# Performance work log

Measured on AMD Instinct MI355X. Metric: run time of the kernel, lower is better.

Reference implementation:

```python
import jax, jax.numpy as jnp
import numpy as np

N, S, E, H = 4, 4096, 1024, 16
D = E // H  # 64


def setup_inputs() -> dict:
    key = jax.random.key(0)
    ks = jax.random.split(key, 6)
    scale = 0.02
    x = jax.random.normal(ks[0], (N, S, E), dtype=jnp.float32)
    Wq = jax.random.normal(ks[1], (E, E), dtype=jnp.float32) * scale
    Wk = jax.random.normal(ks[2], (E, E), dtype=jnp.float32) * scale
    Wv = jax.random.normal(ks[3], (E, E), dtype=jnp.float32) * scale
    Wo = jax.random.normal(ks[4], (E, E), dtype=jnp.float32) * scale
    bo = jax.random.normal(ks[5], (E,), dtype=jnp.float32) * scale
    return {"x": x, "Wq": Wq, "Wk": Wk, "Wv": Wv, "Wo": Wo, "bo": bo}


def reference(x, Wq, Wk, Wv, Wo, bo):
    n, s, _ = x.shape
    # torch nn.Linear(bias=False): y = x @ W.T  (W stored as [out, in])
    q = (x @ Wq.T).reshape(n, s, H, D).transpose(0, 2, 1, 3)  # (N, H, S, D)
    k = (x @ Wk.T).reshape(n, s, H, D).transpose(0, 2, 1, 3)  # (N, H, S, D)
    v = (x @ Wv.T).reshape(n, s, H, D).transpose(0, 2, 1, 3)  # (N, H, S, D)
    # Faithful to source: einsum subscripts applied to the PERMUTED (N,H,S,D)
    # tensors, so label q->H, h->S. energy: (N, H, H, S)
    energy = jnp.einsum('nqhd,nkhd->nqkh', q, k)
    attention = jax.nn.softmax(energy / (D ** 0.5), axis=3)
    # 'nqkh,nvhd->nqhd': k and v are independently summed free indices
    out = jnp.einsum('nqkh,nvhd->nqhd', attention, v).reshape(n, s, E)  # (N,S,E)
    return out @ Wo.T + bo
```

## Files before the change

### kernel.cpp

```cpp
#include <hip/hip_runtime.h>
#include <stdint.h>

typedef unsigned short u16;
typedef unsigned int   u32;
typedef __attribute__((ext_vector_type(8))) short short8;
typedef __attribute__((ext_vector_type(4))) float f32x4;
typedef __attribute__((ext_vector_type(8))) u16   u16x8;

static constexpr size_t NX = (size_t)4 * 4096 * 1024;
static constexpr size_t NW = (size_t)1024 * 1024;

static constexpr size_t OFF_XB   = 0;
static constexpr size_t OFF_EN   = 0;
static constexpr size_t OFF_QK   = 33554432;
static constexpr size_t OFF_WQB  = 100663296;
static constexpr size_t OFF_WKB  = 102760448;
static constexpr size_t OFF_WOB  = 104857600;
static constexpr size_t OFF_WVST = 106954752;
static constexpr size_t OFF_VS   = 107216896;
static constexpr size_t OFF_GMAX = 111411200;
static constexpr size_t OFF_INVZ = 111415296;
static constexpr size_t OFF_ST   = 111419392;

static __device__ __forceinline__ u16 f2bf(float f) {
    u32 u = __builtin_bit_cast(u32, f);
    u += 0x7fffu + ((u >> 16) & 1u);
    return (u16)(u >> 16);
}
static __device__ __forceinline__ float bf2f(u16 v) {
    u32 u = ((u32)v) << 16;
    return __builtin_bit_cast(float, u);
}

#if __has_builtin(__builtin_amdgcn_global_load_lds)
#define HAVE_GLOAD_LDS 1
static __device__ __forceinline__ void gload_lds16(const void* g, void* l) {
    __builtin_amdgcn_global_load_lds(
        (__attribute__((address_space(1))) void*)(uintptr_t)g,
        (__attribute__((address_space(3))) void*)(uintptr_t)l,
        16, 0, 0);
}
#endif

#if __has_builtin(__builtin_amdgcn_sched_barrier)
#define SCHED_FENCE() __builtin_amdgcn_sched_barrier(0)
#else
#define SCHED_FENCE()
#endif

__global__ __launch_bounds__(256)
void cvt_kernel(const float* __restrict__ x, const float* __restrict__ wq,
                const float* __restrict__ wk, const float* __restrict__ wo,
                u16* __restrict__ xb, u16* __restrict__ wqb,
                u16* __restrict__ wkb, u16* __restrict__ wob)
{
    size_t i = ((size_t)blockIdx.x * 256 + threadIdx.x) * 8;
    const float* s; u16* dst; size_t o;
    if (i < NX) { s = x; dst = xb; o = i; }
    else {
        size_t r = i - NX;
        int w = (int)(r >> 20);
        o = r & (NW - 1);
        s   = (w == 0) ? wq  : (w == 1) ? wk  : wo;
        dst = (w == 0) ? wqb : (w == 1) ? wkb : wob;
    }
    f32x4 a = *(const f32x4*)&s[o];
    f32x4 c = *(const f32x4*)&s[o + 4];
    u16x8 v;
    v[0]=f2bf(a[0]); v[1]=f2bf(a[1]); v[2]=f2bf(a[2]); v[3]=f2bf(a[3]);
    v[4]=f2bf(c[0]); v[5]=f2bf(c[1]); v[6]=f2bf(c[2]); v[7]=f2bf(c[3]);
    *(u16x8*)&dst[o] = v;
}

__global__ __launch_bounds__(256)
void wvst_kernel(const float* __restrict__ Wv, u16* __restrict__ Bvs)
{
    int idx = blockIdx.x * 256 + threadIdx.x;
    int d = idx >> 10;
    int e = idx & 1023;
    float s = 0.f;
    #pragma unroll
    for (int h = 0; h < 16; ++h) s += Wv[(size_t)(h * 64 + d) * 1024 + e];
    Bvs[(size_t)d * 1024 + e] = f2bf(s);
}

__global__ __launch_bounds__(512, 2)
void gemm_qk(const u16* __restrict__ A, const u16* __restrict__ Bw,
             u16* __restrict__ C, int M, int N, int K, int lognbx)
{
    __shared__ u16 lds[65536];
    const int tid  = threadIdx.x;
    const int wave = tid >> 6;
    const int lane = tid & 63;

    const int nwg = gridDim.x;
    const int swz = ((int)blockIdx.x & 7) * (nwg >> 3) + ((int)blockIdx.x >> 3);
    const long col0 = (long)(swz & ((1 << lognbx) - 1)) * 256;
    const long row0 = (long)(swz >> lognbx) * 256;

    const int wr2 = wave >> 2;
    const int wc2 = wave & 3;
    const int fr  = lane & 15;
    const int kq  = lane >> 4;
    const int rxor = fr & 7;

    const int t255  = tid & 255;
    const int halfA = tid >> 8;
    const int gAsrc = (t255 & 7) ^ ((t255 >> 3) & 7);
    const u16* sA = A + (size_t)(row0 + halfA * 128 + (t255 >> 3)) * K + gAsrc * 8;
    const int dA = halfA * 8192 + t255 * 8;

    const int u  = (tid & 127) | ((tid >> 1) & 128);
    const int bh = (tid >> 7) & 1;
    const int gBsrc = (u & 7) ^ ((u >> 3) & 7);
    const u16* sB = Bw + (size_t)(col0 + bh * 128 + (u >> 3)) * K + gBsrc * 8;
    const int dB = bh * 8192 + u * 8;

    auto STAGE = [&](int buf, int k0) {
        #pragma unroll
        for (int l = 0; l < 4; ++l) {
#ifdef HAVE_GLOAD_LDS
            gload_lds16(sA + (size_t)l * 32 * K + k0, &lds[buf * 16384 + dA + l * 2048]);
            gload_lds16(sB + (size_t)l * 32 * K + k0, &lds[32768 + buf * 16384 + dB + l * 2048]);
#else
            *(short8*)&lds[buf * 16384 + dA + l * 2048] =
                *(const short8*)(sA + (size_t)l * 32 * K + k0);
            *(short8*)&lds[32768 + buf * 16384 + dB + l * 2048] =
                *(const short8*)(sB + (size_t)l * 32 * K + k0);
#endif
        }
    };

    f32x4 acc[8][4] = {};

    STAGE(0, 0);
    __syncthreads();

    const int nt = K >> 6;
    for (int t = 0; t < nt; ++t) {
        const int cur = t & 1;
        const int base  = cur * 16384;
        const int bbase = 32768 + cur * 16384;

        short8 af[4][2], bf[4][2];
        #pragma unroll
        for (int m = 0; m < 4; ++m) {
            const int row = wr2 * 128 + m * 16 + fr;
            #pragma unroll
            for (int kk = 0; kk < 2; ++kk)
                af[m][kk] = *(const short8*)&lds[base + row * 64 + (((kk << 2) | kq) ^ rxor) * 8];
        }
        #pragma unroll
        for (int n = 0; n < 4; ++n) {
            const int col = wc2 * 64 + n * 16 + fr;
            #pragma unroll
            for (int kk = 0; kk < 2; ++kk)
                bf[n][kk] = *(const short8*)&lds[bbase + col * 64 + (((kk << 2) | kq) ^ rxor) * 8];
        }
        if (t + 1 < nt) STAGE(cur ^ 1, (t + 1) << 6);
        SCHED_FENCE();
        __builtin_amdgcn_s_barrier();

        __builtin_amdgcn_s_setprio(1);
        #pragma unroll
        for (int kk = 0; kk < 2; ++kk)
            #pragma unroll
            for (int m = 0; m < 4; ++m)
                #pragma unroll
                for (int n = 0; n < 2; ++n)
                    acc[m][n] = __builtin_amdgcn_mfma_f32_16x16x32_bf16(af[m][kk], bf[n][kk], acc[m][n], 0, 0, 0);
        __builtin_amdgcn_s_setprio(0);
        __builtin_amdgcn_s_barrier();

        __builtin_amdgcn_s_setprio(1);
        #pragma unroll
        for (int kk = 0; kk < 2; ++kk)
            #pragma unroll
            for (int m = 0; m < 4; ++m)
                #pragma unroll
                for (int n = 2; n < 4; ++n)
                    acc[m][n] = __builtin_amdgcn_mfma_f32_16x16x32_bf16(af[m][kk], bf[n][kk], acc[m][n], 0, 0, 0);
        __builtin_amdgcn_s_setprio(0);

        short8 ag[4][2];
        #pragma unroll
        for (int m = 0; m < 4; ++m) {
            const int row = wr2 * 128 + 64 + m * 16 + fr;
            #pragma unroll
            for (int kk = 0; kk < 2; ++kk)
                ag[m][kk] = *(const short8*)&lds[base + row * 64 + (((kk << 2) | kq) ^ rxor) * 8];
        }
        SCHED_FENCE();
        __builtin_amdgcn_s_barrier();

        __builtin_amdgcn_s_setprio(1);
        #pragma unroll
        for (int kk = 0; kk < 2; ++kk)
            #pragma unroll
            for (int m = 0; m < 4; ++m)
                #pragma unroll
                for (int n = 0; n < 2; ++n)
                    acc[m + 4][n] = __builtin_amdgcn_mfma_f32_16x16x32_bf16(ag[m][kk], bf[n][kk], acc[m + 4][n], 0, 0, 0);
        __builtin_amdgcn_s_setprio(0);
        __builtin_amdgcn_s_barrier();

        __builtin_amdgcn_s_setprio(1);
        #pragma unroll
        for (int kk = 0; kk < 2; ++kk)
            #pragma unroll
            for (int m = 0; m < 4; ++m)
                #pragma unroll
                for (int n = 2; n < 4; ++n)
                    acc[m + 4][n] = __builtin_amdgcn_mfma_f32_16x16x32_bf16(ag[m][kk], bf[n][kk], acc[m + 4][n], 0, 0, 0);
        __builtin_amdgcn_s_setprio(0);

        __syncthreads();
    }

    #pragma unroll
    for (int m = 0; m < 8; ++m) {
        #pragma unroll
        for (int n = 0; n < 4; ++n) {
            long gr = row0 + wr2 * 128 + m * 16 + kq * 4;
            long gc = col0 + wc2 * 64 + n * 16 + fr;
            #pragma unroll
            for (int j = 0; j < 4; ++j)
                C[(gr + j) * N + gc] = f2bf(acc[m][n][j]);
        }
    }
}

__global__ __launch_bounds__(256)
void gemm_vs(const u16* __restrict__ A, const u16* __restrict__ Bw,
             u16* __restrict__ C)
{
    __shared__ u16 lsA[2][64 * 32];
    __shared__ u16 lsB[2][64 * 32];
    const int tid  = threadIdx.x;
    const int wave = tid >> 6;
    const int lane = tid & 63;
    const long row0 = (long)blockIdx.x * 64;
    const int wr = (wave >> 1) * 32;
    const int wc = (wave & 1) * 32;
    const int fr = lane & 15;
    const int k8 = (lane >> 4) * 8;

    f32x4 acc[2][2] = {};
    const int c0 = tid;
    const u16* pa = &A [(row0 + (c0 >> 2)) * 1024 + (c0 & 3) * 8];
    const u16* pb = &Bw[((size_t)(c0 >> 2)) * 1024 + (c0 & 3) * 8];

    auto STAGE = [&](int buf, int k0) {
#ifdef HAVE_GLOAD_LDS
        gload_lds16(pa + k0, &lsA[buf][wave * 512]);
        gload_lds16(pb + k0, &lsB[buf][wave * 512]);
#else
        *(short8*)&lsA[buf][(size_t)c0 * 8] = *(const short8*)(pa + k0);
        *(short8*)&lsB[buf][(size_t)c0 * 8] = *(const short8*)(pb + k0);
#endif
    };

    STAGE(0, 0);
    __syncthreads();
    for (int t = 0; t < 32; ++t) {
        const int cur = t & 1;
        if (t + 1 < 32) STAGE(cur ^ 1, (t + 1) << 5);
        short8 af[2], bf[2];
        #pragma unroll
        for (int m = 0; m < 2; ++m)
            af[m] = *(const short8*)&lsA[cur][(wr + m * 16 + fr) * 32 + k8];
        #pragma unroll
        for (int n = 0; n < 2; ++n)
            bf[n] = *(const short8*)&lsB[cur][(wc + n * 16 + fr) * 32 + k8];
        #pragma unroll
        for (int m = 0; m < 2; ++m)
            #pragma unroll
            for (int n = 0; n < 2; ++n)
                acc[m][n] = __builtin_amdgcn_mfma_f32_16x16x32_bf16(af[m], bf[n], acc[m][n], 0, 0, 0);
        __syncthreads();
    }

    const int orow = (lane >> 4) * 4;
    #pragma unroll
    for (int m = 0; m < 2; ++m) {
        #pragma unroll
        for (int n = 0; n < 2; ++n) {
            long gr = row0 + wr + m * 16 + orow;
            int  gc = wc + n * 16 + fr;
            #pragma unroll
            for (int j = 0; j < 4; ++j)
                C[(gr + j) * 64 + gc] = f2bf(acc[m][n][j]);
        }
    }
}

__global__ __launch_bounds__(256)
void energy_kernel(const u16* __restrict__ QKb, float* __restrict__ E)
{
    const int lane = threadIdx.x & 63;
    const size_t site = (size_t)blockIdx.x * 4 + (threadIdx.x >> 6);
    const u16* qrow = QKb + site * 2048;
    const int hh = lane & 15;
    const int kg = (lane >> 4) * 8;
    short8 a0 = *(const short8*)&qrow[hh * 64 + kg];
    short8 a1 = *(const short8*)&qrow[hh * 64 + 32 + kg];
    short8 b0 = *(const short8*)&qrow[1024 + hh * 64 + kg];
    short8 b1 = *(const short8*)&qrow[1024 + hh * 64 + 32 + kg];
    f32x4 acc = {};
    acc = __builtin_amdgcn_mfma_f32_16x16x32_bf16(a0, b0, acc, 0, 0, 0);
    acc = __builtin_amdgcn_mfma_f32_16x16x32_bf16(a1, b1, acc, 0, 0, 0);
    float* out = E + site * 256;
    const int ib = (lane >> 4) * 4;
    #pragma unroll
    for (int r = 0; r < 4; ++r)
        out[(ib + r) * 16 + hh] = acc[r];
}

__global__ __launch_bounds__(256)
void stats_part(const float* __restrict__ E, float* __restrict__ pmax,
                float* __restrict__ psum)
{
    const int b = blockIdx.x, p = threadIdx.x;
    const float* e = E + (size_t)b * 64 * 256 + p;
    float m = -3.4e38f;
    float buf[64];
    #pragma unroll 8
    for (int s = 0; s < 64; ++s) {
        float v = e[(size_t)s * 256];
        buf[s] = v;
        m = fmaxf(m, v);
    }
    float z = 0.f;
    #pragma unroll 8
    for (int s = 0; s < 64; ++s) z += __expf((buf[s] - m) * 0.125f);
    pmax[b * 256 + p] = m;
    psum[b * 256 + p] = z;
}
__global__ __launch_bounds__(256)
void stats_comb(const float* __restrict__ pmax, const float* __restrict__ psum,
                float* __restrict__ gmax, float* __restrict__ invZ)
{
    const int n = blockIdx.x, p = threadIdx.x;
    float m = -3.4e38f;
    #pragma unroll 8
    for (int c = 0; c < 64; ++c) m = fmaxf(m, pmax[(n * 64 + c) * 256 + p]);
    float z = 0.f;
    #pragma unroll 8
    for (int c = 0; c < 64; ++c)
        z += psum[(n * 64 + c) * 256 + p] * __expf((pmax[(n * 64 + c) * 256 + p] - m) * 0.125f);
    gmax[n * 256 + p] = m;
    invZ[n * 256 + p] = 1.0f / z;
}

__global__ __launch_bounds__(256)
void g_kernel(const u16* __restrict__ Vsb, const u16* __restrict__ Wob,
              float* __restrict__ G)
{
    __shared__ u16 lA[64 * 64];
    __shared__ u16 lB[256 * 64];
    const int tid = threadIdx.x;
    const int wave = tid >> 6, lane = tid & 63;
    const int op = blockIdx.x, uc = blockIdx.y, sl = blockIdx.z;

    {
        const int j = tid >> 2;
        const size_t srow = (size_t)16 * (64 * uc + j) + sl;
        #pragma unroll
        for (int h = 0; h < 2; ++h) {
            const int g = (tid & 3) + h * 4;
            u16x8 v = *(const u16x8*)&Vsb[srow * 64 + g * 8];
            *(u16x8*)&lA[j * 64 + ((g ^ (j & 7)) * 8)] = v;
        }
    }
    {
        const size_t o = (size_t)op * 256 + tid;
        #pragma unroll
        for (int g = 0; g < 8; ++g) {
            u16x8 v = *(const u16x8*)&Wob[o * 1024 + 64 * sl + g * 8];
            *(u16x8*)&lB[tid * 64 + ((g ^ (tid & 7)) * 8)] = v;
        }
    }
    __syncthreads();

    const int fr = lane & 15, kq = lane >> 4;
    f32x4 acc[4][4] = {};
    #pragma unroll
    for (int kk = 0; kk < 2; ++kk) {
        short8 af[4], bq[4];
        #pragma unroll
        for (int m = 0; m < 4; ++m) {
            const int j = m * 16 + fr;
            af[m] = *(const short8*)&lA[j * 64 + (((kq + 4 * kk) ^ (j & 7)) * 8)];
        }
        #pragma unroll
        for (int n = 0; n < 4; ++n) {
            const int o = wave * 64 + n * 16 + fr;
            bq[n] = *(const short8*)&lB[o * 64 + (((kq + 4 * kk) ^ (o & 7)) * 8)];
        }
        #pragma unroll
        for (int m = 0; m < 4; ++m)
            #pragma unroll
            for (int n = 0; n < 4; ++n)
                acc[m][n] = __builtin_amdgcn_mfma_f32_16x16x32_bf16(af[m], bq[n], acc[m][n], 0, 0, 0);
    }

    #pragma unroll
    for (int m = 0; m < 4; ++m) {
        #pragma unroll
        for (int n = 0; n < 4; ++n) {
            const int ocol = op * 256 + wave * 64 + n * 16 + fr;
            #pragma unroll
            for (int jj = 0; jj < 4; ++jj) {
                const int j = m * 16 + kq * 4 + jj;
                G[((size_t)16 * (64 * uc + j) + sl) * 1024 + ocol] = acc[m][n][jj];
            }
        }
    }
}

__global__ __launch_bounds__(256)
void comb_kernel(const float* __restrict__ En, const float* __restrict__ gmax,
                 const float* __restrict__ invZ, const float* __restrict__ G,
                 const float* __restrict__ bo, float* __restrict__ out)
{
    __shared__ float sm[256], sz[256], sa[256];
    const int b = blockIdx.x;
    const int n = b >> 8, c = b & 255;
    const int t = threadIdx.x;
    sm[t] = gmax[n * 256 + t];
    sz[t] = invZ[n * 256 + t];
    __syncthreads();
    {
        const int sl = t >> 4, i = t & 15;
        const float* e = En + ((size_t)n * 4096 + c * 16 + sl) * 256 + i * 16;
        float a = 0.f;
        #pragma unroll
        for (int j = 0; j < 16; ++j)
            a += __expf((e[j] - sm[i * 16 + j]) * 0.125f) * sz[i * 16 + j];
        sa[sl * 16 + i] = a;
    }
    __syncthreads();

    const int o0 = t * 4;
    const float* gp = G + ((size_t)n * 4096 + c * 16) * 1024 + o0;
    f32x4 g[16];
    #pragma unroll
    for (int sl = 0; sl < 16; ++sl) g[sl] = *(const f32x4*)&gp[(size_t)sl * 1024];
    const f32x4 b4 = *(const f32x4*)&bo[o0];
    #pragma unroll
    for (int i = 0; i < 16; ++i) {
        f32x4 acc = b4;
        #pragma unroll
        for (int sl = 0; sl < 16; ++sl) {
            const float a = sa[sl * 16 + i];
            acc[0] += a * g[sl][0];
            acc[1] += a * g[sl][1];
            acc[2] += a * g[sl][2];
            acc[3] += a * g[sl][3];
        }
        *(f32x4*)&out[((size_t)n * 4096 + i * 256 + c) * 1024 + o0] = acc;
    }
}

extern "C" void kernel_launch(void* const* d_in, const int* in_sizes, int n_in,
                              void* d_out, int out_size, void* d_ws, size_t ws_size,
                              hipStream_t stream)
{
    const float* x  = (const float*)d_in[0];
    const float* Wq = (const float*)d_in[1];
    const float* Wk = (const float*)d_in[2];
    const float* Wv = (const float*)d_in[3];
    const float* Wo = (const float*)d_in[4];
    const float* bo = (const float*)d_in[5];
    float* out = (float*)d_out;
    char* ws = (char*)d_ws;

    u16*   xb   = (u16*)  (ws + OFF_XB);
    float* En   = (float*)(ws + OFF_EN);
    u16*   QKb  = (u16*)  (ws + OFF_QK);
    float* G    = (float*)(ws + OFF_QK);
    u16*   Wqb  = (u16*)  (ws + OFF_WQB);
    u16*   Wkb  = (u16*)  (ws + OFF_WKB);
    u16*   Wob  = (u16*)  (ws + OFF_WOB);
    u16*   Bvs  = (u16*)  (ws + OFF_WVST);
    u16*   Vsb  = (u16*)  (ws + OFF_VS);
    float* gmax = (float*)(ws + OFF_GMAX);
    float* invZ = (float*)(ws + OFF_INVZ);
    float* pmax = (float*)(ws + OFF_ST);
    float* psum = (float*)(ws + OFF_ST + 262144);

    cvt_kernel <<<9728, 256, 0, stream>>>(x, Wq, Wk, Wo, xb, Wqb, Wkb, Wob);
    wvst_kernel<<<256,  256, 0, stream>>>(Wv, Bvs);

    gemm_qk<<<512, 512, 0, stream>>>(xb, Wqb, QKb, 16384, 2048, 1024, 3);
    gemm_vs<<<256, 256, 0, stream>>>(xb, Bvs, Vsb);

    energy_kernel<<<4096, 256, 0, stream>>>(QKb, En);

    stats_part<<<256, 256, 0, stream>>>(En, pmax, psum);
    stats_comb<<<4,   256, 0, stream>>>(pmax, psum, gmax, invZ);

    g_kernel<<<dim3(4, 16, 16), 256, 0, stream>>>(Vsb, Wob, G);

    comb_kernel<<<1024, 256, 0, stream>>>(En, gmax, invZ, G, bo, out);
}
```

Baseline: 185.3 us.

## Store G intermediate in bf16 and drop intra-iteration barriers in QK GEMM

The G matrix (attention-weight by Wo product) is now written as bf16 instead of fp32 and converted back in the combine kernel, halving the write and read traffic of this large intermediate. Separately, the QK GEMM main loop issues the next-tile prefetch first, loads all A and B fragments up front, and removes the per-quarter s_barrier synchronisations, reordering the MFMAs into three groups. This trades some accuracy in G and higher register pressure in the GEMM for less memory traffic and fewer barriers.

Result: faster. 179.7 us (-3.0%).

```diff
diff --git a/kernel.cpp b/kernel.cpp
--- a/kernel.cpp
+++ b/kernel.cpp
@@ -6,6 +6,7 @@
 typedef __attribute__((ext_vector_type(8))) short short8;
 typedef __attribute__((ext_vector_type(4))) float f32x4;
 typedef __attribute__((ext_vector_type(8))) u16   u16x8;
+typedef __attribute__((ext_vector_type(4))) u16   u16x4;
 
 static constexpr size_t NX = (size_t)4 * 4096 * 1024;
 static constexpr size_t NW = (size_t)1024 * 1024;
@@ -142,7 +143,9 @@
         const int base  = cur * 16384;
         const int bbase = 32768 + cur * 16384;
 
-        short8 af[4][2], bf[4][2];
+        if (t + 1 < nt) STAGE(cur ^ 1, (t + 1) << 6);
+
+        short8 af[4][2], ag[4][2], bf[2][2], bg[2][2];
         #pragma unroll
         for (int m = 0; m < 4; ++m) {
             const int row = wr2 * 128 + m * 16 + fr;
@@ -151,15 +154,20 @@
                 af[m][kk] = *(const short8*)&lds[base + row * 64 + (((kk << 2) | kq) ^ rxor) * 8];
         }
         #pragma unroll
-        for (int n = 0; n < 4; ++n) {
+        for (int n = 0; n < 2; ++n) {
             const int col = wc2 * 64 + n * 16 + fr;
             #pragma unroll
             for (int kk = 0; kk < 2; ++kk)
                 bf[n][kk] = *(const short8*)&lds[bbase + col * 64 + (((kk << 2) | kq) ^ rxor) * 8];
         }
-        if (t + 1 < nt) STAGE(cur ^ 1, (t + 1) << 6);
+        #pragma unroll
+        for (int m = 0; m < 4; ++m) {
+            const int row = wr2 * 128 + 64 + m * 16 + fr;
+            #pragma unroll
+            for (int kk = 0; kk < 2; ++kk)
+                ag[m][kk] = *(const short8*)&lds[base + row * 64 + (((kk << 2) | kq) ^ rxor) * 8];
+        }
         SCHED_FENCE();
-        __builtin_amdgcn_s_barrier();
 
         __builtin_amdgcn_s_setprio(1);
         #pragma unroll
@@ -170,28 +178,15 @@
                 for (int n = 0; n < 2; ++n)
                     acc[m][n] = __builtin_amdgcn_mfma_f32_16x16x32_bf16(af[m][kk], bf[n][kk], acc[m][n], 0, 0, 0);
         __builtin_amdgcn_s_setprio(0);
-        __builtin_amdgcn_s_barrier();
-
-        __builtin_amdgcn_s_setprio(1);
-        #pragma unroll
-        for (int kk = 0; kk < 2; ++kk)
-            #pragma unroll
-            for (int m = 0; m < 4; ++m)
-                #pragma unroll
-                for (int n = 2; n < 4; ++n)
-                    acc[m][n] = __builtin_amdgcn_mfma_f32_16x16x32_bf16(af[m][kk], bf[n][kk], acc[m][n], 0, 0, 0);
-        __builtin_amdgcn_s_setprio(0);
-
-        short8 ag[4][2];
-        #pragma unroll
-        for (int m = 0; m < 4; ++m) {
-            const int row = wr2 * 128 + 64 + m * 16 + fr;
+
+        #pragma unroll
+        for (int n = 0; n < 2; ++n) {
+            const int col = wc2 * 64 + (n + 2) * 16 + fr;
             #pragma unroll
             for (int kk = 0; kk < 2; ++kk)
-                ag[m][kk] = *(const short8*)&lds[base + row * 64 + (((kk << 2) | kq) ^ rxor) * 8];
+                bg[n][kk] = *(const short8*)&lds[bbase + col * 64 + (((kk << 2) | kq) ^ rxor) * 8];
         }
         SCHED_FENCE();
-        __builtin_amdgcn_s_barrier();
 
         __builtin_amdgcn_s_setprio(1);
         #pragma unroll
@@ -201,17 +196,20 @@
                 #pragma unroll
                 for (int n = 0; n < 2; ++n)
                     acc[m + 4][n] = __builtin_amdgcn_mfma_f32_16x16x32_bf16(ag[m][kk], bf[n][kk], acc[m + 4][n], 0, 0, 0);
-        __builtin_amdgcn_s_setprio(0);
-        __builtin_amdgcn_s_barrier();
-
-        __builtin_amdgcn_s_setprio(1);
         #pragma unroll
         for (int kk = 0; kk < 2; ++kk)
             #pragma unroll
             for (int m = 0; m < 4; ++m)
                 #pragma unroll
-                for (int n = 2; n < 4; ++n)
-                    acc[m + 4][n] = __builtin_amdgcn_mfma_f32_16x16x32_bf16(ag[m][kk], bf[n][kk], acc[m + 4][n], 0, 0, 0);
+                for (int n = 0; n < 2; ++n)
+                    acc[m][n + 2] = __builtin_amdgcn_mfma_f32_16x16x32_bf16(af[m][kk], bg[n][kk], acc[m][n + 2], 0, 0, 0);
+        #pragma unroll
+        for (int kk = 0; kk < 2; ++kk)
+            #pragma unroll
+            for (int m = 0; m < 4; ++m)
+                #pragma unroll
+                for (int n = 0; n < 2; ++n)
+                    acc[m + 4][n + 2] = __builtin_amdgcn_mfma_f32_16x16x32_bf16(ag[m][kk], bg[n][kk], acc[m + 4][n + 2], 0, 0, 0);
         __builtin_amdgcn_s_setprio(0);
 
         __syncthreads();
@@ -354,7 +352,7 @@
 
 __global__ __launch_bounds__(256)
 void g_kernel(const u16* __restrict__ Vsb, const u16* __restrict__ Wob,
-              float* __restrict__ G)
+              u16* __restrict__ G)
 {
     __shared__ u16 lA[64 * 64];
     __shared__ u16 lB[256 * 64];
@@ -412,7 +410,7 @@
             #pragma unroll
             for (int jj = 0; jj < 4; ++jj) {
                 const int j = m * 16 + kq * 4 + jj;
-                G[((size_t)16 * (64 * uc + j) + sl) * 1024 + ocol] = acc[m][n][jj];
+                G[((size_t)16 * (64 * uc + j) + sl) * 1024 + ocol] = f2bf(acc[m][n][jj]);
             }
         }
     }
@@ -420,7 +418,7 @@
 
 __global__ __launch_bounds__(256)
 void comb_kernel(const float* __restrict__ En, const float* __restrict__ gmax,
-                 const float* __restrict__ invZ, const float* __restrict__ G,
+                 const float* __restrict__ invZ, const u16* __restrict__ G,
                  const float* __restrict__ bo, float* __restrict__ out)
 {
     __shared__ float sm[256], sz[256], sa[256];
@@ -442,10 +440,14 @@
     __syncthreads();
 
     const int o0 = t * 4;
-    const float* gp = G + ((size_t)n * 4096 + c * 16) * 1024 + o0;
+    const u16* gp = G + ((size_t)n * 4096 + c * 16) * 1024 + o0;
     f32x4 g[16];
     #pragma unroll
-    for (int sl = 0; sl < 16; ++sl) g[sl] = *(const f32x4*)&gp[(size_t)sl * 1024];
+    for (int sl = 0; sl < 16; ++sl) {
+        u16x4 gv = *(const u16x4*)&gp[(size_t)sl * 1024];
+        g[sl][0] = bf2f(gv[0]); g[sl][1] = bf2f(gv[1]);
+        g[sl][2] = bf2f(gv[2]); g[sl][3] = bf2f(gv[3]);
+    }
     const f32x4 b4 = *(const f32x4*)&bo[o0];
     #pragma unroll
     for (int i = 0; i < 16; ++i) {
@@ -478,7 +480,7 @@
     u16*   xb   = (u16*)  (ws + OFF_XB);
     float* En   = (float*)(ws + OFF_EN);
     u16*   QKb  = (u16*)  (ws + OFF_QK);
-    float* G    = (float*)(ws + OFF_QK);
+    u16*   G    = (u16*)  (ws + OFF_QK);
     u16*   Wqb  = (u16*)  (ws + OFF_WQB);
     u16*   Wkb  = (u16*)  (ws + OFF_WKB);
     u16*   Wob  = (u16*)  (ws + OFF_WOB);
```
